# Kernel tuning notes

Hardware: AMD Instinct MI355X
Metric: run time of the kernel (lower is better)

## Reference

```python
import jax, jax.numpy as jnp
import numpy as np

C = 64
SIZE = 448
PATCH = 14
P2 = PATCH * PATCH                 # 196, per-chunk token count
SPLIT = (SIZE * SIZE) // P2        # 1024 chunks
TG = PATCH * 4                     # 56, pooled global resolution
POOL = SIZE // TG                  # 8, exact avg-pool factor
EPS = 1e-5


def setup_inputs() -> dict:
    key = jax.random.key(0)
    ks = jax.random.split(key, 10)
    b = 2
    x = jax.random.normal(ks[0], (b, C, SIZE, SIZE), dtype=jnp.float32)
    s = 1.0 / np.sqrt(C)
    return {
        "x": x,
        "gn_w": jnp.ones((C,), jnp.float32),
        "gn_b": jnp.zeros((C,), jnp.float32),
        "q_w": jax.random.normal(ks[1], (C, C), jnp.float32) * s,
        "q_b": jnp.zeros((C,), jnp.float32),
        "k_w": jax.random.normal(ks[2], (C, C), jnp.float32) * s,
        "k_b": jnp.zeros((C,), jnp.float32),
        "v_w": jax.random.normal(ks[3], (C, C), jnp.float32) * s,
        "v_b": jnp.zeros((C,), jnp.float32),
        "proj_w": jax.random.normal(ks[4], (C, C), jnp.float32) * s,
    }


def _conv1x1(t, W, bias=None):
    out = jnp.einsum('oc,bchw->bohw', W, t)
    if bias is not None:
        out = out + bias[None, :, None, None]
    return out


def _group_norm(x, w, b):
    # GroupNorm(num_groups=1): normalize over (C,H,W) per sample
    mean = x.mean(axis=(1, 2, 3), keepdims=True)
    var = x.var(axis=(1, 2, 3), keepdims=True)
    xn = (x - mean) * jax.lax.rsqrt(var + EPS)
    return xn * w[None, :, None, None] + b[None, :, None, None]


def reference(x, gn_w, gn_b, q_w, q_b, k_w, k_b, v_w, v_b, proj_w):
    b, c, h, w = x.shape
    xn = _group_norm(x, gn_w, gn_b)
    q = _conv1x1(xn, q_w, q_b)
    k = _conv1x1(xn, k_w, k_b)
    v = _conv1x1(xn, v_w, v_b)

    # ---- patch-local attention (channels*chunks as feature dim S) ----
    S = c * SPLIT  # 65536
    qf = q.reshape(b, S, P2)
    kf = k.reshape(b, S, P2)
    vf = v.reshape(b, S, P2)
    wm = jnp.einsum('bsp,bsq->bpq', qf, kf) * (S ** -0.5)  # [b,196,196]
    wm = jax.nn.softmax(wm, axis=2)
    # h[b,s,q'] = sum_k v[b,s,k] * wm[b,q',k]
    hp = jnp.einsum('bsk,bqk->bsq', vf, wm).reshape(b, c, h, w)

    # ---- global pooled attention ----
    pool = lambda t: t.reshape(b, c, TG, POOL, TG, POOL).mean(axis=(3, 5))
    qg = pool(q).reshape(b, c, TG * TG)
    kg = pool(k).reshape(b, c, TG * TG)
    vg = pool(v).reshape(b, c, TG * TG)
    wg = jnp.einsum('bcp,bcq->bpq', qg, kg) * (c ** -0.5)  # [b,3136,3136]
    wg = jax.nn.softmax(wg, axis=2)
    hg = jnp.einsum('bck,bqk->bcq', vg, wg).reshape(b, c, TG, TG)
    hg = jnp.repeat(jnp.repeat(hg, POOL, axis=2), POOL, axis=3)

    h_in = 0.75 * hp + 0.25 * hg
    out = _conv1x1(h_in, proj_w)  # proj_out, no bias
    return x + out
```

## Files before the change

### kernel.cpp

```cpp
#include <hip/hip_runtime.h>

#define NB 2
#define NC 64
#define HW 200704
#define CHW 12845056
#define P2 196
#define NCHUNK 1024
#define NCELL 3136
#define WMN 38416

typedef __attribute__((ext_vector_type(8))) short bfrag;
typedef __attribute__((ext_vector_type(4))) float ffrag;
typedef __attribute__((ext_vector_type(4))) short short4v;
typedef __attribute__((ext_vector_type(4))) float float4v;

#define MFMA16(A,B,C) __builtin_amdgcn_mfma_f32_16x16x32_bf16(A,B,C,0,0,0)

__device__ __forceinline__ short f2bf(float f) {
  unsigned u = __builtin_bit_cast(unsigned, f);
  u = u + 0x7FFFu + ((u >> 16) & 1u);
  return (short)(u >> 16);
}

__global__ __launch_bounds__(64) void k1_stats_pool(
    const float* __restrict__ x, float* __restrict__ xpool, float* __restrict__ partials) {
  int bx = blockIdx.x;
  int batch = bx / (64*56);
  int c = (bx / 56) % 64;
  int pr = bx % 56;
  int l = threadIdx.x;
  const float* xp = x + (size_t)batch*CHW + (size_t)c*HW + pr*8*448;
  float cell = 0.f, s2 = 0.f;
  if (l < 56) {
    #pragma unroll
    for (int r = 0; r < 8; ++r) {
      float4v a = *(const float4v*)(xp + r*448 + l*8);
      float4v b = *(const float4v*)(xp + r*448 + l*8 + 4);
      #pragma unroll
      for (int j = 0; j < 4; ++j) { cell += a[j] + b[j]; s2 += a[j]*a[j] + b[j]*b[j]; }
    }
    xpool[((size_t)batch*64 + c)*NCELL + pr*56 + l] = cell * (1.f/64.f);
  }
  float s1 = (l < 56) ? cell : 0.f;
  #pragma unroll
  for (int m = 1; m < 64; m <<= 1) { s1 += __shfl_xor(s1, m, 64); s2 += __shfl_xor(s2, m, 64); }
  if (l == 0) { partials[bx*2] = s1; partials[bx*2 + 1] = s2; }
}

__global__ __launch_bounds__(256) void k1b_reduce(
    const float* __restrict__ partials, float* __restrict__ stats) {
  __shared__ float red[2][256];
  int t = threadIdx.x;
  for (int b = 0; b < NB; ++b) {
    float s1 = 0.f, s2 = 0.f;
    for (int i = t; i < 3584; i += 256) {
      s1 += partials[(b*3584 + i)*2];
      s2 += partials[(b*3584 + i)*2 + 1];
    }
    red[0][t] = s1; red[1][t] = s2;
    __syncthreads();
    for (int m = 128; m > 0; m >>= 1) {
      if (t < m) { red[0][t] += red[0][t+m]; red[1][t] += red[1][t+m]; }
      __syncthreads();
    }
    if (t == 0) { stats[b*2] = red[0][0]; stats[b*2+1] = red[1][0]; }
    __syncthreads();
  }
}

__global__ __launch_bounds__(256) void k2_qkv(
    const float* __restrict__ x, const float* __restrict__ gnw, const float* __restrict__ gnb,
    const float* __restrict__ qw, const float* __restrict__ qb,
    const float* __restrict__ kw, const float* __restrict__ kb,
    const float* __restrict__ vw, const float* __restrict__ vb,
    const float* __restrict__ stats,
    short* __restrict__ qx, short* __restrict__ kx, short* __restrict__ vnat) {
  __shared__ __attribute__((aligned(16))) short xnt[256*72];
  int bx = blockIdx.x;
  int batch = bx / 784;
  int px0 = (bx % 784) * 256;
  int t = threadIdx.x;
  float s1 = stats[batch*2], s2 = stats[batch*2+1];
  float mean = s1 * (1.f/CHW);
  float rstd = rsqrtf(s2*(1.f/CHW) - mean*mean + 1e-5f);
  for (int it = 0; it < 64; it += 4) {
    float vv[4];
    #pragma unroll
    for (int r = 0; r < 4; ++r) {
      float v = x[(size_t)batch*CHW + (size_t)(it+r)*HW + px0 + t];
      vv[r] = (v - mean) * rstd * gnw[it+r] + gnb[it+r];
    }
    short4v s;
    #pragma unroll
    for (int r = 0; r < 4; ++r) s[r] = f2bf(vv[r]);
    *(short4v*)(xnt + t*72 + it) = s;
  }
  __syncthreads();
  int l = t & 63, w = t >> 6, li = l & 15, q_ = l >> 4;
  bfrag bfr[4][2];
  #pragma unroll
  for (int nn = 0; nn < 4; ++nn) {
    int row = (w*4 + nn)*16 + li;
    bfr[nn][0] = *(const bfrag*)(xnt + row*72 + q_*8);
    bfr[nn][1] = *(const bfrag*)(xnt + row*72 + 32 + q_*8);
  }
  const float* Ws[3] = {qw, kw, vw};
  const float* Bs[3] = {qb, kb, vb};
  for (int T = 0; T < 3; ++T) {
    ffrag acc[4][4];
    #pragma unroll
    for (int mt = 0; mt < 4; ++mt) {
      bfrag a0, a1;
      const float* wp = Ws[T] + (mt*16 + li)*64;
      #pragma unroll
      for (int j = 0; j < 8; ++j) { a0[j] = f2bf(wp[q_*8 + j]); a1[j] = f2bf(wp[32 + q_*8 + j]); }
      #pragma unroll
      for (int nn = 0; nn < 4; ++nn) {
        ffrag z = {0.f,0.f,0.f,0.f};
        z = MFMA16(a0, bfr[nn][0], z);
        z = MFMA16(a1, bfr[nn][1], z);
        acc[mt][nn] = z;
      }
    }
    if (T < 2) {
      short* dstb = (T == 0 ? qx : kx) + (size_t)batch*HW*64;
      #pragma unroll
      for (int nn = 0; nn < 4; ++nn) {
        int px = px0 + (w*4 + nn)*16 + li;
        #pragma unroll
        for (int mt = 0; mt < 4; ++mt) {
          float4v bias = *(const float4v*)(Bs[T] + mt*16 + q_*4);
          short4v s;
          #pragma unroll
          for (int r = 0; r < 4; ++r) s[r] = f2bf(acc[mt][nn][r] + bias[r]);
          *(short4v*)(dstb + (size_t)px*64 + mt*16 + q_*4) = s;
        }
      }
    } else {
      #pragma unroll
      for (int nn = 0; nn < 4; ++nn) {
        int px = px0 + (w*4 + nn)*16 + li;
        #pragma unroll
        for (int mt = 0; mt < 4; ++mt) {
          float4v bias = *(const float4v*)(Bs[T] + mt*16 + q_*4);
          #pragma unroll
          for (int r = 0; r < 4; ++r) {
            int c = mt*16 + q_*4 + r;
            vnat[((size_t)batch*64 + c)*HW + px] = f2bf(acc[mt][nn][r] + bias[r]);
          }
        }
      }
    }
  }
}

__global__ __launch_bounds__(256) void k2a_pool_qkv(
    const float* __restrict__ xpool, const float* __restrict__ stats,
    const float* __restrict__ gnw, const float* __restrict__ gnb,
    const float* __restrict__ qw, const float* __restrict__ qb,
    const float* __restrict__ kw, const float* __restrict__ kb,
    const float* __restrict__ vw, const float* __restrict__ vb,
    short* __restrict__ qgt, short* __restrict__ kgt, short* __restrict__ vgn) {
  __shared__ float xs[64][64];
  int bx = blockIdx.x;
  int batch = bx / 49;
  int j0 = (bx % 49) * 64;
  int t = threadIdx.x;
  float s1 = stats[batch*2], s2 = stats[batch*2+1];
  float mean = s1 * (1.f/CHW);
  float rstd = rsqrtf(s2*(1.f/CHW) - mean*mean + 1e-5f);
  #pragma unroll
  for (int it = 0; it < 16; ++it) {
    int idx = t + it*256;
    int c = idx >> 6, jl = idx & 63;
    float v = xpool[((size_t)batch*64 + c)*NCELL + j0 + jl];
    xs[c][jl] = (v - mean)*rstd*gnw[c] + gnb[c];
  }
  __syncthreads();
  int jl = t & 63;
  int og = (t >> 6) * 16;
  int j = j0 + jl;
  for (int T = 0; T < 3; ++T) {
    const float* W  = (T==0 ? qw : (T==1 ? kw : vw));
    const float* Bv = (T==0 ? qb : (T==1 ? kb : vb));
    float o16[16];
    #pragma unroll
    for (int oo = 0; oo < 16; ++oo) o16[oo] = Bv[og+oo];
    for (int c = 0; c < 64; ++c) {
      float xv = xs[c][jl];
      #pragma unroll
      for (int oo = 0; oo < 16; ++oo) o16[oo] += W[(og+oo)*64 + c] * xv;
    }
    if (T < 2) {
      short* dst = (T==0 ? qgt : kgt) + ((size_t)batch*NCELL + j)*64 + og;
      #pragma unroll
      for (int oo = 0; oo < 16; oo += 4) {
        short4v s;
        #pragma unroll
        for (int r = 0; r < 4; ++r) s[r] = f2bf(o16[oo+r]);
        *(short4v*)(dst + oo) = s;
      }
    } else {
      #pragma unroll
      for (int oo = 0; oo < 16; ++oo)
        vgn[((size_t)batch*64 + og + oo)*NCELL + j] = f2bf(o16[oo]);
    }
  }
}

__global__ __launch_bounds__(512) void k3_wm(
    const short* __restrict__ qx, const short* __restrict__ kx, float* __restrict__ wmacc) {
  int bx = blockIdx.x;
  int batch = bx >> 6;
  int slab = bx & 63;
  int t = threadIdx.x;
  int l = t & 63, w = t >> 6, li = l & 15, q_ = l >> 4;
  int wm_ = w >> 2, wn = w & 3;
  int m0 = wm_ * 7, mcnt = wm_ ? 6 : 7;
  int nt0 = wn ? 4 + (wn-1)*3 : 0, ncnt = wn ? 3 : 4;
  ffrag acc[7][4];
  #pragma unroll
  for (int i = 0; i < 7; ++i)
    #pragma unroll
    for (int j = 0; j < 4; ++j) acc[i][j] = (ffrag){0.f,0.f,0.f,0.f};
  const short* qbase = qx + (size_t)batch*HW*64;
  const short* kbase = kx + (size_t)batch*HW*64;
  for (int c8 = 0; c8 < 16; ++c8) {
    int chunk = slab*16 + c8;
    const short* qc = qbase + (size_t)chunk*P2*64;
    const short* kc = kbase + (size_t)chunk*P2*64;
    #pragma unroll
    for (int ks = 0; ks < 2; ++ks) {
      int koff = ks*32 + q_*8;
      bfrag af[7], bf[4];
      #pragma unroll
      for (int mi = 0; mi < 7; ++mi) if (mi < mcnt)
        af[mi] = *(const bfrag*)(qc + (size_t)((m0+mi)*16 + li)*64 + koff);
      #pragma unroll
      for (int ni = 0; ni < 4; ++ni) if (ni < ncnt)
        bf[ni] = *(const bfrag*)(kc + (size_t)((nt0+ni)*16 + li)*64 + koff);
      #pragma unroll
      for (int mi = 0; mi < 7; ++mi) if (mi < mcnt)
        #pragma unroll
        for (int ni = 0; ni < 4; ++ni) if (ni < ncnt)
          acc[mi][ni] = MFMA16(af[mi], bf[ni], acc[mi][ni]);
    }
  }
  float* wdst = wmacc + (size_t)batch*WMN;
  #pragma unroll
  for (int mi = 0; mi < 7; ++mi) if (mi < mcnt)
    #pragma unroll
    for (int ni = 0; ni < 4; ++ni) if (ni < ncnt) {
      int qcol = (nt0+ni)*16 + li;
      if (qcol < 196)
        #pragma unroll
        for (int r = 0; r < 4; ++r) {
          int prow = (m0+mi)*16 + q_*4 + r;
          if (prow < 196) atomicAdd(wdst + prow*196 + qcol, acc[mi][ni][r]);
        }
    }
}

__global__ __launch_bounds__(64) void k4_softmax(
    const float* __restrict__ wmacc, short* __restrict__ P) {
  int bx = blockIdx.x;
  int batch = bx / 208;
  int p = bx % 208;
  int l = threadIdx.x;
  short* prow = P + ((size_t)batch*208 + p)*224;
  if (p >= 196) { for (int j = l; j < 224; j += 64) prow[j] = 0; return; }
  const float* src = wmacc + (size_t)batch*WMN + p*196;
  float v[4]; float mx = -1e30f;
  #pragma unroll
  for (int i = 0; i < 4; ++i) {
    int q = l + i*64;
    v[i] = (q < 196) ? src[q]*(1.f/256.f) : -1e30f;
    mx = fmaxf(mx, v[i]);
  }
  #pragma unroll
  for (int m = 1; m < 64; m <<= 1) mx = fmaxf(mx, __shfl_xor(mx, m, 64));
  float s = 0.f;
  #pragma unroll
  for (int i = 0; i < 4; ++i) { v[i] = __expf(v[i] - mx); s += v[i]; }
  #pragma unroll
  for (int m = 1; m < 64; m <<= 1) s += __shfl_xor(s, m, 64);
  float inv = 1.f / s;
  #pragma unroll
  for (int i = 0; i < 4; ++i) {
    int q = l + i*64;
    if (q < 224) prow[q] = (q < 196) ? f2bf(v[i]*inv) : (short)0;
  }
}

__global__ __launch_bounds__(256) void k5_gattn(
    const short* __restrict__ qgt, const short* __restrict__ kgt,
    const short* __restrict__ vgn, float* __restrict__ hgt) {
  __shared__ __attribute__((aligned(16))) short Pl[4][16][72];
  __shared__ __attribute__((aligned(16))) float alph[4][16];
  __shared__ __attribute__((aligned(16))) float lsum[4][16];
  int bx = blockIdx.x;
  int batch = bx / 49;
  int t = threadIdx.x;
  int w = t >> 6, l = t & 63, li = l & 15, q_ = l >> 4;
  int i0 = (bx % 49)*64 + w*16;
  const short* qg = qgt + (size_t)batch*NCELL*64;
  const short* kg = kgt + (size_t)batch*NCELL*64;
  const short* vg = vgn + (size_t)batch*64*NCELL;
  bfrag bq0 = *(const bfrag*)(qg + (size_t)(i0+li)*64 + q_*8);
  bfrag bq1 = *(const bfrag*)(qg + (size_t)(i0+li)*64 + 32 + q_*8);
  float m_run = -1e30f, l_run = 0.f;
  ffrag oa[4];
  #pragma unroll
  for (int i = 0; i < 4; ++i) oa[i] = (ffrag){0.f,0.f,0.f,0.f};
  for (int jt = 0; jt < 49; ++jt) {
    int j0 = jt*64;
    ffrag st[4];
    #pragma unroll
    for (int mt = 0; mt < 4; ++mt) {
      bfrag a0 = *(const bfrag*)(kg + (size_t)(j0 + mt*16 + li)*64 + q_*8);
      bfrag a1 = *(const bfrag*)(kg + (size_t)(j0 + mt*16 + li)*64 + 32 + q_*8);
      ffrag z = {0.f,0.f,0.f,0.f};
      z = MFMA16(a0, bq0, z);
      z = MFMA16(a1, bq1, z);
      st[mt] = z;
    }
    float mx = -1e30f;
    #pragma unroll
    for (int mt = 0; mt < 4; ++mt)
      #pragma unroll
      for (int r = 0; r < 4; ++r) { st[mt][r] *= 0.125f; mx = fmaxf(mx, st[mt][r]); }
    mx = fmaxf(mx, __shfl_xor(mx, 16, 64));
    mx = fmaxf(mx, __shfl_xor(mx, 32, 64));
    float m_new = fmaxf(m_run, mx);
    float alpha = __expf(m_run - m_new);
    float ps = 0.f;
    short4v pk[4];
    #pragma unroll
    for (int mt = 0; mt < 4; ++mt)
      #pragma unroll
      for (int r = 0; r < 4; ++r) { float e = __expf(st[mt][r] - m_new); ps += e; pk[mt][r] = f2bf(e); }
    ps += __shfl_xor(ps, 16, 64);
    ps += __shfl_xor(ps, 32, 64);
    l_run = l_run*alpha + ps;
    m_run = m_new;
    #pragma unroll
    for (int mt = 0; mt < 4; ++mt) *(short4v*)(&Pl[w][li][mt*16 + q_*4]) = pk[mt];
    alph[w][li] = alpha;
    __syncthreads();
    float4v al = *(const float4v*)(&alph[w][q_*4]);
    #pragma unroll
    for (int nt = 0; nt < 4; ++nt)
      #pragma unroll
      for (int r = 0; r < 4; ++r) oa[nt][r] *= al[r];
    #pragma unroll
    for (int ks = 0; ks < 2; ++ks) {
      bfrag a = *(const bfrag*)(&Pl[w][li][ks*32 + q_*8]);
      #pragma unroll
      for (int nt = 0; nt < 4; ++nt) {
        bfrag b = *(const bfrag*)(vg + (size_t)(nt*16 + li)*NCELL + j0 + ks*32 + q_*8);
        oa[nt] = MFMA16(a, b, oa[nt]);
      }
    }
    __syncthreads();
  }
  lsum[w][li] = l_run;
  __syncthreads();
  float4v lv = *(const float4v*)(&lsum[w][q_*4]);
  float* dst = hgt + (size_t)batch*NCELL*64;
  #pragma unroll
  for (int r = 0; r < 4; ++r) {
    float inv = 1.f / lv[r];
    int i = i0 + q_*4 + r;
    #pragma unroll
    for (int nt = 0; nt < 4; ++nt) dst[(size_t)i*64 + nt*16 + li] = oa[nt][r] * inv;
  }
}

__global__ __launch_bounds__(256) void k6_hp_proj(
    const short* __restrict__ vnat, const short* __restrict__ P,
    const float* __restrict__ hgt, const float* __restrict__ projw,
    const float* __restrict__ x, float* __restrict__ out) {
  __shared__ __attribute__((aligned(16))) short vch[64*224];
  __shared__ __attribute__((aligned(16))) short hl[208*72];
  int bx = blockIdx.x;
  int batch = bx >> 10;
  int chunk = bx & 1023;
  int t = threadIdx.x;
  const short* vsrc = vnat + (size_t)batch*64*HW + chunk*P2;
  for (int idx = t; idx < 3136; idx += 256) {
    int c = idx / 49, po = idx % 49;
    *(short4v*)(vch + c*224 + po*4) = *(const short4v*)(vsrc + (size_t)c*HW + po*4);
  }
  for (int idx = t; idx < 448; idx += 256) {
    int c = idx / 7, po = idx % 7;
    *(short4v*)(vch + c*224 + 196 + po*4) = (short4v){0,0,0,0};
  }
  __syncthreads();
  int l = t & 63, w = t >> 6, li = l & 15, q_ = l >> 4;
  int nt0 = w ? 4 + (w-1)*3 : 0;
  int ncnt = w ? 3 : 4;
  const short* Pb = P + (size_t)batch*208*224;
  ffrag acc[4][4];
  #pragma unroll
  for (int i = 0; i < 4; ++i)
    #pragma unroll
    for (int j = 0; j < 4; ++j) acc[i][j] = (ffrag){0.f,0.f,0.f,0.f};
  #pragma unroll
  for (int ks = 0; ks < 7; ++ks) {
    int koff = ks*32 + q_*8;
    bfrag av[4];
    #pragma unroll
    for (int mt = 0; mt < 4; ++mt) av[mt] = *(const bfrag*)(vch + (mt*16 + li)*224 + koff);
    #pragma unroll
    for (int ni = 0; ni < 4; ++ni) if (ni < ncnt) {
      bfrag bp = *(const bfrag*)(Pb + (size_t)((nt0+ni)*16 + li)*224 + koff);
      #pragma unroll
      for (int mt = 0; mt < 4; ++mt) acc[mt][ni] = MFMA16(av[mt], bp, acc[mt][ni]);
    }
  }
  const float* hgb = hgt + (size_t)batch*NCELL*64;
  #pragma unroll
  for (int ni = 0; ni < 4; ++ni) if (ni < ncnt) {
    int pp = (nt0+ni)*16 + li;
    if (pp < 196) {
      int g = chunk*P2 + pp;
      int hh = g / 448, ww_ = g % 448;
      int cell = (hh >> 3)*56 + (ww_ >> 3);
      #pragma unroll
      for (int mt = 0; mt < 4; ++mt) {
        float4v hgv = *(const float4v*)(hgb + (size_t)cell*64 + mt*16 + q_*4);
        short4v s;
        #pragma unroll
        for (int r = 0; r < 4; ++r) s[r] = f2bf(0.75f*acc[mt][ni][r] + 0.25f*hgv[r]);
        *(short4v*)(hl + pp*72 + mt*16 + q_*4) = s;
      }
    }
  }
  __syncthreads();
  ffrag acc2[4][4];
  #pragma unroll
  for (int i = 0; i < 4; ++i)
    #pragma unroll
    for (int j = 0; j < 4; ++j) acc2[i][j] = (ffrag){0.f,0.f,0.f,0.f};
  #pragma unroll
  for (int ks = 0; ks < 2; ++ks) {
    bfrag aw[4];
    #pragma unroll
    for (int mt = 0; mt < 4; ++mt) {
      const float* wp = projw + (mt*16 + li)*64 + ks*32 + q_*8;
      #pragma unroll
      for (int j = 0; j < 8; ++j) aw[mt][j] = f2bf(wp[j]);
    }
    #pragma unroll
    for (int ni = 0; ni < 4; ++ni) if (ni < ncnt) {
      bfrag bh = *(const bfrag*)(hl + ((nt0+ni)*16 + li)*72 + ks*32 + q_*8);
      #pragma unroll
      for (int mt = 0; mt < 4; ++mt) acc2[mt][ni] = MFMA16(aw[mt], bh, acc2[mt][ni]);
    }
  }
  const float* xb = x + (size_t)batch*CHW;
  float* ob = out + (size_t)batch*CHW;
  #pragma unroll
  for (int ni = 0; ni < 4; ++ni) if (ni < ncnt) {
    int pp = (nt0+ni)*16 + li;
    if (pp < 196) {
      int g = chunk*P2 + pp;
      #pragma unroll
      for (int mt = 0; mt < 4; ++mt)
        #pragma unroll
        for (int r = 0; r < 4; ++r) {
          int o = mt*16 + q_*4 + r;
          ob[(size_t)o*HW + g] = xb[(size_t)o*HW + g] + acc2[mt][ni][r];
        }
    }
  }
}

extern "C" void kernel_launch(void* const* d_in, const int* in_sizes, int n_in,
                              void* d_out, int out_size, void* d_ws, size_t ws_size,
                              hipStream_t stream) {
  (void)in_sizes; (void)n_in; (void)out_size; (void)ws_size;
  const float* x   = (const float*)d_in[0];
  const float* gnw = (const float*)d_in[1];
  const float* gnb = (const float*)d_in[2];
  const float* qw  = (const float*)d_in[3];
  const float* qb  = (const float*)d_in[4];
  const float* kw  = (const float*)d_in[5];
  const float* kb  = (const float*)d_in[6];
  const float* vw  = (const float*)d_in[7];
  const float* vb  = (const float*)d_in[8];
  const float* pw  = (const float*)d_in[9];
  float* out = (float*)d_out;
  char* ws = (char*)d_ws;

  short* qx    = (short*)(ws + 0);
  short* kx    = (short*)(ws + 51380224);
  short* vnat  = (short*)(ws + 102760448);
  float* xpool = (float*)(ws + 154140672);
  short* qgt   = (short*)(ws + 155746304);
  short* kgt   = (short*)(ws + 156549120);
  short* vgn   = (short*)(ws + 157351936);
  float* hgt   = (float*)(ws + 158154752);
  short* P     = (short*)(ws + 159760384);
  float* wmacc = (float*)(ws + 159946752);
  float* stats = (float*)(ws + 160254080);
  float* partials = (float*)(ws + 159760384);

  hipMemsetAsync(ws + 159946752, 0, 307328, stream);
  k1_stats_pool<<<dim3(NB*64*56), dim3(64),  0, stream>>>(x, xpool, partials);
  k1b_reduce   <<<dim3(1),        dim3(256), 0, stream>>>(partials, stats);
  k2_qkv       <<<dim3(NB*784),   dim3(256), 0, stream>>>(x, gnw, gnb, qw, qb, kw, kb, vw, vb, stats, qx, kx, vnat);
  k2a_pool_qkv <<<dim3(NB*49),    dim3(256), 0, stream>>>(xpool, stats, gnw, gnb, qw, qb, kw, kb, vw, vb, qgt, kgt, vgn);
  k3_wm        <<<dim3(NB*64),    dim3(512), 0, stream>>>(qx, kx, wmacc);
  k4_softmax   <<<dim3(NB*208),   dim3(64),  0, stream>>>(wmacc, P);
  k5_gattn     <<<dim3(NB*49),    dim3(256), 0, stream>>>(qgt, kgt, vgn, hgt);
  k6_hp_proj   <<<dim3(NB*1024),  dim3(256), 0, stream>>>(vnat, P, hgt, pw, x, out);
}
```

Before: 698.3 us.

## Alias LDS buffers and stage output through shared memory for vectorized stores

Merges the V chunk buffer and the hidden buffer into one aliased LDS allocation, which reduces shared memory per block and may raise occupancy. The V row stride is padded from 224 to 232 to cut LDS bank conflicts. The final residual add now goes through LDS in two channel halves, so global loads and stores of x and out become contiguous float4 accesses instead of scattered scalar ones. The cost is extra barriers and the zeroing of padding rows.

```diff
diff --git a/kernel.cpp b/kernel.cpp
--- a/kernel.cpp
+++ b/kernel.cpp
@@ -380,8 +380,10 @@
     const short* __restrict__ vnat, const short* __restrict__ P,
     const float* __restrict__ hgt, const float* __restrict__ projw,
     const float* __restrict__ x, float* __restrict__ out) {
-  __shared__ __attribute__((aligned(16))) short vch[64*224];
-  __shared__ __attribute__((aligned(16))) short hl[208*72];
+  __shared__ __attribute__((aligned(16))) short smem[208*72];
+  short* vch = smem;
+  short* hl  = smem;
+  float* fs  = (float*)smem;
   int bx = blockIdx.x;
   int batch = bx >> 10;
   int chunk = bx & 1023;
@@ -389,11 +391,11 @@
   const short* vsrc = vnat + (size_t)batch*64*HW + chunk*P2;
   for (int idx = t; idx < 3136; idx += 256) {
     int c = idx / 49, po = idx % 49;
-    *(short4v*)(vch + c*224 + po*4) = *(const short4v*)(vsrc + (size_t)c*HW + po*4);
+    *(short4v*)(vch + c*232 + po*4) = *(const short4v*)(vsrc + (size_t)c*HW + po*4);
   }
   for (int idx = t; idx < 448; idx += 256) {
     int c = idx / 7, po = idx % 7;
-    *(short4v*)(vch + c*224 + 196 + po*4) = (short4v){0,0,0,0};
+    *(short4v*)(vch + c*232 + 196 + po*4) = (short4v){0,0,0,0};
   }
   __syncthreads();
   int l = t & 63, w = t >> 6, li = l & 15, q_ = l >> 4;
@@ -410,7 +412,7 @@
     int koff = ks*32 + q_*8;
     bfrag av[4];
     #pragma unroll
-    for (int mt = 0; mt < 4; ++mt) av[mt] = *(const bfrag*)(vch + (mt*16 + li)*224 + koff);
+    for (int mt = 0; mt < 4; ++mt) av[mt] = *(const bfrag*)(vch + (mt*16 + li)*232 + koff);
     #pragma unroll
     for (int ni = 0; ni < 4; ++ni) if (ni < ncnt) {
       bfrag bp = *(const bfrag*)(Pb + (size_t)((nt0+ni)*16 + li)*224 + koff);
@@ -418,6 +420,7 @@
       for (int mt = 0; mt < 4; ++mt) acc[mt][ni] = MFMA16(av[mt], bp, acc[mt][ni]);
     }
   }
+  __syncthreads();
   const float* hgb = hgt + (size_t)batch*NCELL*64;
   #pragma unroll
   for (int ni = 0; ni < 4; ++ni) if (ni < ncnt) {
@@ -436,6 +439,10 @@
       }
     }
   }
+  for (int idx = t; idx < 216; idx += 256) {
+    int rr = 196 + idx/18, cc = (idx%18)*4;
+    *(short4v*)(hl + rr*72 + cc) = (short4v){0,0,0,0};
+  }
   __syncthreads();
   ffrag acc2[4][4];
   #pragma unroll
@@ -458,21 +465,35 @@
       for (int mt = 0; mt < 4; ++mt) acc2[mt][ni] = MFMA16(aw[mt], bh, acc2[mt][ni]);
     }
   }
+  __syncthreads();
   const float* xb = x + (size_t)batch*CHW;
   float* ob = out + (size_t)batch*CHW;
   #pragma unroll
-  for (int ni = 0; ni < 4; ++ni) if (ni < ncnt) {
-    int pp = (nt0+ni)*16 + li;
-    if (pp < 196) {
-      int g = chunk*P2 + pp;
-      #pragma unroll
-      for (int mt = 0; mt < 4; ++mt)
-        #pragma unroll
-        for (int r = 0; r < 4; ++r) {
-          int o = mt*16 + q_*4 + r;
-          ob[(size_t)o*HW + g] = xb[(size_t)o*HW + g] + acc2[mt][ni][r];
+  for (int h = 0; h < 2; ++h) {
+    #pragma unroll
+    for (int ni = 0; ni < 4; ++ni) if (ni < ncnt) {
+      int pp = (nt0+ni)*16 + li;
+      if (pp < 196) {
+        #pragma unroll
+        for (int mt = 0; mt < 2; ++mt) {
+          #pragma unroll
+          for (int r = 0; r < 4; ++r)
+            fs[(mt*16 + q_*4 + r)*204 + pp] = acc2[h*2 + mt][ni][r];
         }
-    }
+      }
+    }
+    __syncthreads();
+    for (int idx = t; idx < 32*49; idx += 256) {
+      int c = idx / 49, po = idx % 49;
+      size_t off = (size_t)(h*32 + c)*HW + (size_t)chunk*P2 + po*4;
+      float4v xv = *(const float4v*)(xb + off);
+      float4v fv = *(const float4v*)(fs + c*204 + po*4);
+      float4v o;
+      #pragma unroll
+      for (int r = 0; r < 4; ++r) o[r] = xv[r] + fv[r];
+      *(float4v*)(ob + off) = o;
+    }
+    __syncthreads();
   }
 }
 
```

Measured after the change: 682.3 us. 1.02x faster.
